# Kernel optimization log

Hardware: AMD Instinct MI355X
Metric: run time of the kernel (lower is better)

Reference implementation:

```python
import jax, jax.numpy as jnp
import numpy as np
from math import sqrt

D_MODEL = 1024
N_HEADS = 16
FF_MULT = 4
MAX_DIST = 512
LN_EPS = 1e-5


def layer_norm(x, g, b):
    mu = jnp.mean(x, axis=-1, keepdims=True)
    var = jnp.var(x, axis=-1, keepdims=True)
    return (x - mu) * jax.lax.rsqrt(var + LN_EPS) * g + b


def setup_inputs() -> dict:
    key = jax.random.key(0)
    ks = jax.random.split(key, 10)
    D, H, F = D_MODEL, N_HEADS, D_MODEL * FF_MULT
    s = 0.02
    return {
        "x": jax.random.normal(ks[0], (2, 2048, D), dtype=jnp.float32),
        "w_qkv": jax.random.normal(ks[1], (D, 3 * D), dtype=jnp.float32) * s,
        "b_qkv": jnp.zeros((3 * D,), jnp.float32),
        "w_out": jax.random.normal(ks[2], (D, D), dtype=jnp.float32) * s,
        "b_out": jnp.zeros((D,), jnp.float32),
        "rel_bias": jax.random.normal(ks[3], (2 * MAX_DIST + 1, H), dtype=jnp.float32) * s,
        "g1": jnp.ones((D,), jnp.float32),
        "beta1": jnp.zeros((D,), jnp.float32),
        "w1": jax.random.normal(ks[4], (D, F), dtype=jnp.float32) * s,
        "b1": jnp.zeros((F,), jnp.float32),
        "w2": jax.random.normal(ks[5], (F, D), dtype=jnp.float32) * s,
        "b2": jnp.zeros((D,), jnp.float32),
        "g2": jnp.ones((D,), jnp.float32),
        "beta2": jnp.zeros((D,), jnp.float32),
    }


def reference(x, w_qkv, b_qkv, w_out, b_out, rel_bias, g1, beta1, w1, b1, w2, b2, g2, beta2):
    B, T, D = x.shape
    H = N_HEADS
    hd = D // H
    qkv = x @ w_qkv + b_qkv                      # [B,T,3D]
    q, k, v = jnp.split(qkv, 3, axis=-1)
    # [B,H,T,hd]
    q = q.reshape(B, T, H, hd).transpose(0, 2, 1, 3)
    k = k.reshape(B, T, H, hd).transpose(0, 2, 1, 3)
    v = v.reshape(B, T, H, hd).transpose(0, 2, 1, 3)
    scores = jnp.einsum("bhqd,bhkd->bhqk", q, k) / sqrt(hd)
    # relative position bias: gather from table [2*max_dist+1, H]
    rel = jnp.clip(jnp.arange(T)[None, :] - jnp.arange(T)[:, None], -MAX_DIST, MAX_DIST) + MAX_DIST
    bias = rel_bias[rel].transpose(2, 0, 1)       # [H,T,T]
    attn = jax.nn.softmax(scores + bias[None], axis=-1)
    out = jnp.einsum("bhqk,bhkd->bhqd", attn, v).transpose(0, 2, 1, 3).reshape(B, T, D)
    out = out @ w_out + b_out                     # dropout inactive (eval)
    x2 = layer_norm(x + out, g1, beta1)
    ff = jax.nn.gelu(x2 @ w1 + b1, approximate=False) @ w2 + b2
    x3 = layer_norm(x2 + ff, g2, beta2)
    return (x3, attn)
```

## Files before the change

kernel.cpp:

```cpp
#include <hip/hip_runtime.h>
#include <hip/hip_bf16.h>
#include <cstdint>
#include <cstddef>

#define DEVFN static __device__ __forceinline__

typedef __attribute__((ext_vector_type(8))) short bf16x8;
typedef __attribute__((ext_vector_type(4))) float f32x4;

#define WAITVM(N) asm volatile("s_waitcnt vmcnt(" #N ")" ::: "memory")
#define WAITLGKM() asm volatile("s_waitcnt lgkmcnt(0)" ::: "memory")
#define BAR() __builtin_amdgcn_s_barrier()

DEVFN float exp2f_fast(float x) { return __builtin_amdgcn_exp2f(x); }

DEVFN ushort f2bf(float f) {
  uint32_t u = __float_as_uint(f);
  return (ushort)((u + 0x7fffu + ((u >> 16) & 1u)) >> 16);
}

DEVFN void gl_lds16(const void* g, void* l) {
  __builtin_amdgcn_global_load_lds(
      (const __attribute__((address_space(1))) void*)g,
      (__attribute__((address_space(3))) void*)l, 16, 0, 0);
}

DEVFN float wred_sum(float v) {
#pragma unroll
  for (int o = 32; o; o >>= 1) v += __shfl_xor(v, o);
  return v;
}


__global__ __launch_bounds__(256) void pack_bf16(const float* __restrict__ in,
                                                 ushort* __restrict__ out) {
  size_t i = ((size_t)blockIdx.x * 256 + threadIdx.x) * 4;
  float4 v = *(const float4*)&in[i];
  ushort4 u = make_ushort4(f2bf(v.x), f2bf(v.y), f2bf(v.z), f2bf(v.w));
  *(ushort4*)&out[i] = u;
}

__global__ __launch_bounds__(256) void wtrans(const float* __restrict__ in,
                                              ushort* __restrict__ out,
                                              int K, int N) {
  __shared__ float tile[32][33];
  int n0 = blockIdx.x * 32, k0 = blockIdx.y * 32;
  int tid = threadIdx.x;
#pragma unroll
  for (int i = 0; i < 4; ++i) {
    int idx = tid + i * 256;
    int r = idx >> 5, c = idx & 31;
    tile[r][c] = in[(size_t)(k0 + r) * N + n0 + c];
  }
  __syncthreads();
#pragma unroll
  for (int i = 0; i < 4; ++i) {
    int idx = tid + i * 256;
    int r = idx >> 5, c = idx & 31;
    out[(size_t)(n0 + r) * K + k0 + c] = f2bf(tile[c][r]);
  }
}

__global__ __launch_bounds__(256) void pack_vT(const ushort* __restrict__ qkv,
                                               ushort* __restrict__ vT) {
  __shared__ ushort tile[64][72];
  int bh = blockIdx.y, b = bh >> 4, h = bh & 15;
  int t0 = blockIdx.x * 64;
  int tid = threadIdx.x;
#pragma unroll
  for (int i = 0; i < 16; ++i) {
    int idx = tid + i * 256;
    int r = idx >> 6, c = idx & 63;
    tile[r][c] = qkv[(size_t)(b * 2048 + t0 + r) * 3072 + 2048 + h * 64 + c];
  }
  __syncthreads();
#pragma unroll
  for (int i = 0; i < 16; ++i) {
    int idx = tid + i * 256;
    int d = idx >> 6, t = idx & 63;
    vT[((size_t)bh * 64 + d) * 2048 + t0 + t] = tile[t][d];
  }
}


template <bool GELU, bool STF32, bool STBF16>
__global__ __launch_bounds__(256)
void gemm128(const ushort* __restrict__ A, int lda,
             const ushort* __restrict__ BT, int ldb,
             const float* __restrict__ bias,
             float* __restrict__ Cf, ushort* __restrict__ Cb, int ldc, int K,
             size_t cstride) {
  __shared__ ushort lsa[128 * 64];
  __shared__ ushort lsb[128 * 64];
  const int tid = threadIdx.x;
  const int lane = tid & 63;
  const int wv = tid >> 6;
  const int wr = (wv >> 1) * 64, wc = (wv & 1) * 64;
  const size_t kStart = (size_t)blockIdx.z * K;
  const ushort* Ab = A + (size_t)blockIdx.y * 128 * lda + kStart;
  const ushort* Bb = BT + (size_t)blockIdx.x * 128 * ldb + kStart;
  f32x4 acc[4][4] = {};
  int rowS[4], slotS[4];
#pragma unroll
  for (int i = 0; i < 4; ++i) {
    int idx = tid + i * 256;
    rowS[i] = idx >> 3;
    slotS[i] = (idx & 7) ^ (rowS[i] & 7);
  }
  for (int kt = 0; kt < K; kt += 64) {
    __syncthreads();
#pragma unroll
    for (int i = 0; i < 4; ++i) {
      gl_lds16(Ab + (size_t)rowS[i] * lda + kt + slotS[i] * 8, &lsa[(tid + i * 256) * 8]);
      gl_lds16(Bb + (size_t)rowS[i] * ldb + kt + slotS[i] * 8, &lsb[(tid + i * 256) * 8]);
    }
    asm volatile("s_waitcnt vmcnt(0)" ::: "memory");
    __syncthreads();
#pragma unroll
    for (int kk = 0; kk < 2; ++kk) {
      bf16x8 af[4], bfr[4];
      const int g = kk * 4 + (lane >> 4);
#pragma unroll
      for (int m = 0; m < 4; ++m) {
        int r = wr + m * 16 + (lane & 15);
        af[m] = *(const bf16x8*)&lsa[r * 64 + ((g ^ (r & 7)) * 8)];
      }
#pragma unroll
      for (int n = 0; n < 4; ++n) {
        int r = wc + n * 16 + (lane & 15);
        bfr[n] = *(const bf16x8*)&lsb[r * 64 + ((g ^ (r & 7)) * 8)];
      }
#pragma unroll
      for (int m = 0; m < 4; ++m)
#pragma unroll
        for (int n = 0; n < 4; ++n)
          acc[m][n] = __builtin_amdgcn_mfma_f32_16x16x32_bf16(af[m], bfr[n], acc[m][n], 0, 0, 0);
    }
  }
  const int rb = blockIdx.y * 128 + wr + ((lane >> 4) << 2);
  const int cb = blockIdx.x * 128 + wc + (lane & 15);
  float* Cfz = Cf + (size_t)blockIdx.z * cstride;
  ushort* Cbz = Cb + (size_t)blockIdx.z * cstride;
#pragma unroll
  for (int m = 0; m < 4; ++m)
#pragma unroll
    for (int n = 0; n < 4; ++n) {
      int col = cb + n * 16;
      float bv = bias ? bias[col] : 0.0f;
#pragma unroll
      for (int i = 0; i < 4; ++i) {
        int row = rb + m * 16 + i;
        float v = acc[m][n][i] + bv;
        if (GELU) v = 0.5f * v * (1.0f + erff(v * 0.70710678f));
        if (STF32) Cfz[(size_t)row * ldc + col] = v;
        if (STBF16) Cbz[(size_t)row * ldc + col] = f2bf(v);
      }
    }
}


DEVFN void attn_bid2(int& qb, int& bh, int& hf) {
  int lin = blockIdx.x;
  int xcd = lin & 7;
  int idx = lin >> 3;
  int orig = xcd * 128 + idx;
  hf = orig & 1;
  qb = (orig >> 1) & 15;
  bh = orig >> 5;
}

__global__ __launch_bounds__(256, 4)
void attn_den(const ushort* __restrict__ qkv, const float* __restrict__ rel_bias,
              float* __restrict__ lsum) {
  __shared__ ushort lsk[2][64 * 64];
  __shared__ float extb[1034];
  const int tid = threadIdx.x;
  const int lane = tid & 63;
  const int wv = tid >> 6;
  const int hi = lane >> 4;
  const int lo = lane & 15;
  int qb, bh, hf;
  attn_bid2(qb, bh, hf);
  const int b = bh >> 4, h = bh & 15;
  const int q0 = qb * 128;
  const int t0 = hf * 16;
  const ushort* qp = qkv + (size_t)b * 2048 * 3072 + h * 64;
  const ushort* kp = qp + 1024;
  const float C_SC = 0.18033688011f;
  ushort* lsq = (ushort*)lsk;

  for (int i = tid; i < 1034; i += 256) {
    int j = i - 3;
    j = j < 0 ? 0 : (j > 1024 ? 1024 : j);
    extb[i] = rel_bias[j * 16 + h] * 1.44269504f;
  }
#pragma unroll
  for (int i = 0; i < 4; ++i) {
    int idx = tid + i * 256;
    int row = idx >> 3;
    int slot = (idx & 7) ^ (row & 7);
    gl_lds16(qp + (size_t)(q0 + row) * 3072 + slot * 8, &lsq[idx * 8]);
  }
  WAITVM(0);
  WAITLGKM();
  BAR();
  bf16x8 qf[2][2];
#pragma unroll
  for (int mq = 0; mq < 2; ++mq)
#pragma unroll
    for (int kk = 0; kk < 2; ++kk) {
      int r = wv * 32 + mq * 16 + lo;
      int g = kk * 4 + hi;
      qf[mq][kk] = *(const bf16x8*)&lsq[r * 64 + ((g ^ (r & 7)) * 8)];
    }
  WAITLGKM();
  BAR();

  const int r0 = tid >> 3;
  const int sl0 = (tid & 7) ^ (r0 & 7);
  const int r1 = (tid + 256) >> 3;
  const int sl1 = ((tid + 256) & 7) ^ (r1 & 7);
  auto stageK = [&](int t, int buf) {
    gl_lds16(kp + (size_t)(t * 64 + r0) * 3072 + sl0 * 8, &lsk[buf][tid * 8]);
    gl_lds16(kp + (size_t)(t * 64 + r1) * 3072 + sl1 * 8, &lsk[buf][(tid + 256) * 8]);
  };

  float l_part[2] = {0.0f, 0.0f};
  stageK(t0, 0);
  for (int t = t0; t < t0 + 16; ++t) {
    if (t < t0 + 15) {
      stageK(t + 1, (t + 1) & 1);
      WAITVM(2);
    } else {
      WAITVM(0);
    }
    BAR();
    f32x4 sacc[4][2] = {};
    __builtin_amdgcn_s_setprio(1);
#pragma unroll
    for (int kk = 0; kk < 2; ++kk) {
      const int g = kk * 4 + hi;
      bf16x8 ak[4];
#pragma unroll
      for (int mk = 0; mk < 4; ++mk) {
        int r = mk * 16 + lo;
        ak[mk] = *(const bf16x8*)&lsk[t & 1][r * 64 + ((g ^ (r & 7)) * 8)];
      }
#pragma unroll
      for (int mk = 0; mk < 4; ++mk)
#pragma unroll
        for (int mq = 0; mq < 2; ++mq)
          sacc[mk][mq] =
              __builtin_amdgcn_mfma_f32_16x16x32_bf16(ak[mk], qf[mq][kk], sacc[mk][mq], 0, 0, 0);
    }
    __builtin_amdgcn_s_setprio(0);
    const bool farR = (t * 64) >= q0 + 640;
    const bool farL = (t * 64 + 63) <= q0 - 512;
    if (farR || farL) {
      const float bc = farR ? extb[3 + 1024] : extb[3];
#pragma unroll
      for (int mq = 0; mq < 2; ++mq) {
        float s = 0.0f;
#pragma unroll
        for (int mk = 0; mk < 4; ++mk)
#pragma unroll
          for (int i = 0; i < 4; ++i)
            s += exp2f_fast(fmaf(sacc[mk][mq][i], C_SC, bc));
        l_part[mq] += s;
      }
    } else {
      const int kbase = t * 64 + hi * 4;
      const int qr = q0 + wv * 32 + lo;
#pragma unroll
      for (int mq = 0; mq < 2; ++mq) {
        float s = 0.0f;
#pragma unroll
        for (int mk = 0; mk < 4; ++mk) {
          int k0 = (kbase + mk * 16) - (qr + mq * 16) + 515;
          k0 = k0 < 0 ? 0 : (k0 > 1030 ? 1030 : k0);
#pragma unroll
          for (int i = 0; i < 4; ++i)
            s += exp2f_fast(fmaf(sacc[mk][mq][i], C_SC, extb[k0 + i]));
        }
        l_part[mq] += s;
      }
    }
    BAR();
  }

#pragma unroll
  for (int mq = 0; mq < 2; ++mq) {
    float l = l_part[mq];
    l += __shfl_xor(l, 16);
    l += __shfl_xor(l, 32);
    if (hi == 0)
      lsum[(size_t)hf * 65536 + (size_t)bh * 2048 + q0 + wv * 32 + mq * 16 + lo] = l;
  }
}

__global__ __launch_bounds__(256, 3)
void attn_pv2(const ushort* __restrict__ qkv, const ushort* __restrict__ vT,
              const float* __restrict__ rel_bias, const float* __restrict__ lsum,
              float* __restrict__ attn, float* __restrict__ opart) {
  __shared__ ushort lsk[2][64 * 64];
  __shared__ ushort lsv[2][64 * 64];
  __shared__ ushort lsp[128 * 64];
  __shared__ float extb[1034];
  const int tid = threadIdx.x;
  const int lane = tid & 63;
  const int wv = tid >> 6;
  const int hi = lane >> 4;
  const int lo = lane & 15;
  int qb, bh, hf;
  attn_bid2(qb, bh, hf);
  const int b = bh >> 4, h = bh & 15;
  const int q0 = qb * 128;
  const int t0 = hf * 16;
  const ushort* qp = qkv + (size_t)b * 2048 * 3072 + h * 64;
  const ushort* kp = qp + 1024;
  const ushort* vp = vT + (size_t)bh * 64 * 2048;
  float* attnb = attn + (size_t)bh * 2048 * 2048;
  const float C_SC = 0.18033688011f;

  for (int i = tid; i < 1034; i += 256) {
    int j = i - 3;
    j = j < 0 ? 0 : (j > 1024 ? 1024 : j);
    extb[i] = rel_bias[j * 16 + h] * 1.44269504f;
  }
#pragma unroll
  for (int i = 0; i < 4; ++i) {
    int idx = tid + i * 256;
    int row = idx >> 3;
    int slot = (idx & 7) ^ (row & 7);
    gl_lds16(qp + (size_t)(q0 + row) * 3072 + slot * 8, &lsp[idx * 8]);
  }
  WAITVM(0);
  WAITLGKM();
  BAR();
  bf16x8 qf[2][2];
#pragma unroll
  for (int mq = 0; mq < 2; ++mq)
#pragma unroll
    for (int kk = 0; kk < 2; ++kk) {
      int r = wv * 32 + mq * 16 + lo;
      int g = kk * 4 + hi;
      qf[mq][kk] = *(const bf16x8*)&lsp[r * 64 + ((g ^ (r & 7)) * 8)];
    }
  WAITLGKM();
  BAR();

  float il[2];
#pragma unroll
  for (int mq = 0; mq < 2; ++mq) {
    size_t qi = (size_t)bh * 2048 + q0 + wv * 32 + mq * 16 + lo;
    il[mq] = 1.0f / (lsum[qi] + lsum[qi + 65536]);
  }

  const int r0 = tid >> 3;
  const int sl0 = (tid & 7) ^ (r0 & 7);
  const int r1 = (tid + 256) >> 3;
  const int sl1 = ((tid + 256) & 7) ^ (r1 & 7);
  auto stageK = [&](int t, int buf) {
    gl_lds16(kp + (size_t)(t * 64 + r0) * 3072 + sl0 * 8, &lsk[buf][tid * 8]);
    gl_lds16(kp + (size_t)(t * 64 + r1) * 3072 + sl1 * 8, &lsk[buf][(tid + 256) * 8]);
  };
  auto stageV = [&](int t, int buf) {
    gl_lds16(vp + (size_t)r0 * 2048 + t * 64 + sl0 * 8, &lsv[buf][tid * 8]);
    gl_lds16(vp + (size_t)r1 * 2048 + t * 64 + sl1 * 8, &lsv[buf][(tid + 256) * 8]);
  };

  f32x4 acc_o[2][4] = {};
  stageK(t0, 0);
  stageV(t0, 0);
  for (int t = t0; t < t0 + 16; ++t) {
    if (t < t0 + 15) {
      stageK(t + 1, (t + 1) & 1);
      stageV(t + 1, (t + 1) & 1);
    }
    if (t == t0) { WAITVM(4); }
    else if (t < t0 + 15) { WAITVM(12); }
    else { WAITVM(8); }
    BAR();
    f32x4 sacc[4][2] = {};
    __builtin_amdgcn_s_setprio(1);
#pragma unroll
    for (int kk = 0; kk < 2; ++kk) {
      const int g = kk * 4 + hi;
      bf16x8 ak[4];
#pragma unroll
      for (int mk = 0; mk < 4; ++mk) {
        int r = mk * 16 + lo;
        ak[mk] = *(const bf16x8*)&lsk[t & 1][r * 64 + ((g ^ (r & 7)) * 8)];
      }
#pragma unroll
      for (int mk = 0; mk < 4; ++mk)
#pragma unroll
        for (int mq = 0; mq < 2; ++mq)
          sacc[mk][mq] =
              __builtin_amdgcn_mfma_f32_16x16x32_bf16(ak[mk], qf[mq][kk], sacc[mk][mq], 0, 0, 0);
    }
    __builtin_amdgcn_s_setprio(0);
    const bool farR = (t * 64) >= q0 + 640;
    const bool farT = farR || ((t * 64 + 63) <= q0 - 512);
    const float bcf = farR ? extb[3 + 1024] : extb[3];
#pragma unroll
    for (int mq = 0; mq < 2; ++mq) {
      const int row = wv * 32 + mq * 16 + lo;
      const float l = il[mq];
#pragma unroll
      for (int mk = 0; mk < 4; ++mk) {
        const int c0 = mk * 16 + hi * 4;
        float p4[4];
        if (farT) {
#pragma unroll
          for (int i = 0; i < 4; ++i)
            p4[i] = exp2f_fast(fmaf(sacc[mk][mq][i], C_SC, bcf)) * l;
        } else {
          int k0 = (t * 64 + c0) - (q0 + row) + 515;
          k0 = k0 < 0 ? 0 : (k0 > 1030 ? 1030 : k0);
#pragma unroll
          for (int i = 0; i < 4; ++i)
            p4[i] = exp2f_fast(fmaf(sacc[mk][mq][i], C_SC, extb[k0 + i])) * l;
        }
        ushort4 u = make_ushort4(f2bf(p4[0]), f2bf(p4[1]), f2bf(p4[2]), f2bf(p4[3]));
        *(ushort4*)&lsp[row * 64 + (((c0 >> 3) ^ (row & 7)) << 3) + (c0 & 7)] = u;
        *(float4*)&attnb[(size_t)(q0 + row) * 2048 + t * 64 + c0] =
            make_float4(p4[0], p4[1], p4[2], p4[3]);
      }
    }
    WAITLGKM();
    BAR();
    __builtin_amdgcn_s_setprio(1);
#pragma unroll
    for (int kk = 0; kk < 2; ++kk) {
      const int g = kk * 4 + hi;
      bf16x8 ap[2], bv2[4];
#pragma unroll
      for (int m = 0; m < 2; ++m) {
        int r = wv * 32 + m * 16 + lo;
        ap[m] = *(const bf16x8*)&lsp[r * 64 + ((g ^ (r & 7)) * 8)];
      }
#pragma unroll
      for (int n = 0; n < 4; ++n) {
        int r = n * 16 + lo;
        bv2[n] = *(const bf16x8*)&lsv[t & 1][r * 64 + ((g ^ (r & 7)) * 8)];
      }
#pragma unroll
      for (int m = 0; m < 2; ++m)
#pragma unroll
        for (int n = 0; n < 4; ++n)
          acc_o[m][n] = __builtin_amdgcn_mfma_f32_16x16x32_bf16(ap[m], bv2[n], acc_o[m][n], 0, 0, 0);
    }
    __builtin_amdgcn_s_setprio(0);
  }

  float* ob = opart + (size_t)hf * 4194304;
#pragma unroll
  for (int m = 0; m < 2; ++m)
#pragma unroll
    for (int n = 0; n < 4; ++n) {
      int col = h * 64 + n * 16 + lo;
#pragma unroll
      for (int i = 0; i < 4; ++i) {
        int row = q0 + wv * 32 + m * 16 + (hi << 2) + i;
        ob[(size_t)(b * 2048 + row) * 1024 + col] = acc_o[m][n][i];
      }
    }
}

__global__ __launch_bounds__(256) void ocomb(const float* __restrict__ opart,
                                             ushort* __restrict__ ctx) {
  size_t i = ((size_t)blockIdx.x * 256 + threadIdx.x) * 4;
  float4 a = *(const float4*)&opart[i];
  float4 c = *(const float4*)&opart[4194304 + i];
  ushort4 u = make_ushort4(f2bf(a.x + c.x), f2bf(a.y + c.y),
                           f2bf(a.z + c.z), f2bf(a.w + c.w));
  *(ushort4*)&ctx[i] = u;
}


__global__ __launch_bounds__(256)
void add_ln(const float* __restrict__ a, const float* __restrict__ r0,
            const float* __restrict__ r1, const float* __restrict__ bias,
            const float* __restrict__ g, const float* __restrict__ be,
            float* __restrict__ outf, ushort* __restrict__ outb) {
  const int tid = threadIdx.x;
  const size_t base = (size_t)blockIdx.x * 1024 + tid * 4;
  float4 va = *(const float4*)&a[base];
  float4 vr = *(const float4*)&r0[base];
  float x0 = va.x + vr.x, x1 = va.y + vr.y, x2 = va.z + vr.z, x3 = va.w + vr.w;
  if (r1) {
    float4 v1 = *(const float4*)&r1[base];
    x0 += v1.x; x1 += v1.y; x2 += v1.z; x3 += v1.w;
  }
  if (bias) {
    float4 vb4 = *(const float4*)&bias[tid * 4];
    x0 += vb4.x; x1 += vb4.y; x2 += vb4.z; x3 += vb4.w;
  }
  float s = x0 + x1 + x2 + x3;
  float s2 = x0 * x0 + x1 * x1 + x2 * x2 + x3 * x3;
  s = wred_sum(s);
  s2 = wred_sum(s2);
  __shared__ float rs[4], rq[4];
  if ((tid & 63) == 0) { rs[tid >> 6] = s; rq[tid >> 6] = s2; }
  __syncthreads();
  s = rs[0] + rs[1] + rs[2] + rs[3];
  s2 = rq[0] + rq[1] + rq[2] + rq[3];
  const float mean = s * (1.0f / 1024.0f);
  const float var = s2 * (1.0f / 1024.0f) - mean * mean;
  const float sc = rsqrtf(var + 1e-5f);
  float4 vg = *(const float4*)&g[tid * 4];
  float4 vb = *(const float4*)&be[tid * 4];
  float y0 = (x0 - mean) * sc * vg.x + vb.x;
  float y1 = (x1 - mean) * sc * vg.y + vb.y;
  float y2 = (x2 - mean) * sc * vg.z + vb.z;
  float y3 = (x3 - mean) * sc * vg.w + vb.w;
  *(float4*)&outf[base] = make_float4(y0, y1, y2, y3);
  if (outb) {
    ushort4 u = make_ushort4(f2bf(y0), f2bf(y1), f2bf(y2), f2bf(y3));
    *(ushort4*)&outb[base] = u;
  }
}


extern "C" void kernel_launch(void* const* d_in, const int* in_sizes, int n_in,
                              void* d_out, int out_size, void* d_ws, size_t ws_size,
                              hipStream_t stream) {
  const float* x     = (const float*)d_in[0];
  const float* w_qkv = (const float*)d_in[1];
  const float* b_qkv = (const float*)d_in[2];
  const float* w_out = (const float*)d_in[3];
  const float* b_out = (const float*)d_in[4];
  const float* relb  = (const float*)d_in[5];
  const float* g1    = (const float*)d_in[6];
  const float* be1   = (const float*)d_in[7];
  const float* w1    = (const float*)d_in[8];
  const float* b1    = (const float*)d_in[9];
  const float* w2    = (const float*)d_in[10];
  const float* b2    = (const float*)d_in[11];
  const float* g2    = (const float*)d_in[12];
  const float* be2   = (const float*)d_in[13];

  float* x3o  = (float*)d_out;
  float* attn = x3o + (size_t)4194304;

  char* w = (char*)d_ws;
  size_t off = 0;
  auto alloc = [&](size_t bytes) {
    void* p = w + off;
    off += (bytes + 255) & ~(size_t)255;
    return p;
  };
  ushort* x_bf   = (ushort*)alloc(4096ull * 1024 * 2);
  ushort* wqkvT  = (ushort*)alloc(3072ull * 1024 * 2);
  ushort* woutT  = (ushort*)alloc(1024ull * 1024 * 2);
  ushort* w1T    = (ushort*)alloc(4096ull * 1024 * 2);
  ushort* w2T    = (ushort*)alloc(1024ull * 4096 * 2);
  ushort* qkv_bf = (ushort*)alloc(4096ull * 3072 * 2);
  ushort* vT     = (ushort*)alloc(32ull * 64 * 2048 * 2);
  ushort* ctx_bf = (ushort*)alloc(4096ull * 1024 * 2);
  float*  lsum   = (float*)alloc(2ull * 32 * 2048 * 4);
  float*  opart  = (float*)alloc(2ull * 4096 * 1024 * 4);
  float*  p0     = (float*)alloc(4096ull * 1024 * 4);
  float*  p1     = (float*)alloc(4096ull * 1024 * 4);
  float*  x2f    = (float*)alloc(4096ull * 1024 * 4);
  ushort* x2bf   = (ushort*)alloc(4096ull * 1024 * 2);
  ushort* ff1_bf = (ushort*)alloc(4096ull * 4096 * 2);

  pack_bf16<<<4096, 256, 0, stream>>>(x, x_bf);
  wtrans<<<dim3(96, 32), 256, 0, stream>>>(w_qkv, wqkvT, 1024, 3072);
  wtrans<<<dim3(32, 32), 256, 0, stream>>>(w_out, woutT, 1024, 1024);
  wtrans<<<dim3(128, 32), 256, 0, stream>>>(w1, w1T, 1024, 4096);
  wtrans<<<dim3(32, 128), 256, 0, stream>>>(w2, w2T, 4096, 1024);

  gemm128<false, false, true><<<dim3(24, 32), 256, 0, stream>>>(
      x_bf, 1024, wqkvT, 1024, b_qkv, nullptr, qkv_bf, 3072, 1024, 0);
  attn_den<<<1024, 256, 0, stream>>>(qkv_bf, relb, lsum);
  pack_vT<<<dim3(32, 32), 256, 0, stream>>>(qkv_bf, vT);
  attn_pv2<<<1024, 256, 0, stream>>>(qkv_bf, vT, relb, lsum, attn, opart);
  ocomb<<<4096, 256, 0, stream>>>(opart, ctx_bf);

  gemm128<false, true, false><<<dim3(8, 32, 2), 256, 0, stream>>>(
      ctx_bf, 1024, woutT, 1024, nullptr, p0, nullptr, 1024, 512,
      (size_t)(p1 - p0));
  add_ln<<<4096, 256, 0, stream>>>(x, p0, p1, b_out, g1, be1, x2f, x2bf);
  gemm128<true, false, true><<<dim3(32, 32), 256, 0, stream>>>(
      x2bf, 1024, w1T, 1024, b1, nullptr, ff1_bf, 4096, 1024, 0);
  gemm128<false, true, false><<<dim3(8, 32, 2), 256, 0, stream>>>(
      ff1_bf, 4096, w2T, 4096, nullptr, p0, nullptr, 1024, 2048,
      (size_t)(p1 - p0));
  add_ln<<<4096, 256, 0, stream>>>(x2f, p0, p1, b2, g2, be2, x3o, nullptr);
}
```

Baseline: 451.1 us.

## Merge prep kernels, fold V transpose into attn_den, store partial outputs as bf16

Folds the x conversion and the four weight transposes into one prep launch. The V transpose now runs as extra blocks inside the attention-denominator kernel, and attn_pv2 writes its two partial outputs in bf16 instead of fp32. These cut launch count and halve the opart write and read traffic. In exchange, partial outputs are rounded to bf16 before they are summed, and attn_den_vt carries an extra shared tile that may lower its occupancy.

```diff
diff --git a/kernel.cpp b/kernel.cpp
--- a/kernel.cpp
+++ b/kernel.cpp
@@ -18,6 +18,7 @@
   uint32_t u = __float_as_uint(f);
   return (ushort)((u + 0x7fffu + ((u >> 16) & 1u)) >> 16);
 }
+DEVFN float bf2f(ushort u) { return __uint_as_float((uint32_t)u << 16); }
 
 DEVFN void gl_lds16(const void* g, void* l) {
   __builtin_amdgcn_global_load_lds(
@@ -32,53 +33,50 @@
 }
 
 
-__global__ __launch_bounds__(256) void pack_bf16(const float* __restrict__ in,
-                                                 ushort* __restrict__ out) {
-  size_t i = ((size_t)blockIdx.x * 256 + threadIdx.x) * 4;
-  float4 v = *(const float4*)&in[i];
-  ushort4 u = make_ushort4(f2bf(v.x), f2bf(v.y), f2bf(v.z), f2bf(v.w));
-  *(ushort4*)&out[i] = u;
-}
-
-__global__ __launch_bounds__(256) void wtrans(const float* __restrict__ in,
-                                              ushort* __restrict__ out,
-                                              int K, int N) {
-  __shared__ float tile[32][33];
-  int n0 = blockIdx.x * 32, k0 = blockIdx.y * 32;
-  int tid = threadIdx.x;
+DEVFN void wtrans_body(const float* __restrict__ in, ushort* __restrict__ out,
+                       int K, int N, int bx, int by, int tid, float* tile ) {
+  int n0 = bx * 32, k0 = by * 32;
 #pragma unroll
   for (int i = 0; i < 4; ++i) {
     int idx = tid + i * 256;
     int r = idx >> 5, c = idx & 31;
-    tile[r][c] = in[(size_t)(k0 + r) * N + n0 + c];
+    tile[r * 33 + c] = in[(size_t)(k0 + r) * N + n0 + c];
   }
   __syncthreads();
 #pragma unroll
   for (int i = 0; i < 4; ++i) {
     int idx = tid + i * 256;
     int r = idx >> 5, c = idx & 31;
-    out[(size_t)(n0 + r) * K + k0 + c] = f2bf(tile[c][r]);
-  }
-}
-
-__global__ __launch_bounds__(256) void pack_vT(const ushort* __restrict__ qkv,
-                                               ushort* __restrict__ vT) {
-  __shared__ ushort tile[64][72];
-  int bh = blockIdx.y, b = bh >> 4, h = bh & 15;
-  int t0 = blockIdx.x * 64;
-  int tid = threadIdx.x;
-#pragma unroll
-  for (int i = 0; i < 16; ++i) {
-    int idx = tid + i * 256;
-    int r = idx >> 6, c = idx & 63;
-    tile[r][c] = qkv[(size_t)(b * 2048 + t0 + r) * 3072 + 2048 + h * 64 + c];
-  }
-  __syncthreads();
-#pragma unroll
-  for (int i = 0; i < 16; ++i) {
-    int idx = tid + i * 256;
-    int d = idx >> 6, t = idx & 63;
-    vT[((size_t)bh * 64 + d) * 2048 + t0 + t] = tile[t][d];
+    out[(size_t)(n0 + r) * K + k0 + c] = f2bf(tile[c * 33 + r]);
+  }
+}
+
+__global__ __launch_bounds__(256)
+void prep(const float* __restrict__ x, ushort* __restrict__ x_bf,
+          const float* __restrict__ w_qkv, ushort* __restrict__ wqkvT,
+          const float* __restrict__ w1, ushort* __restrict__ w1T,
+          const float* __restrict__ w2, ushort* __restrict__ w2T,
+          const float* __restrict__ w_out, ushort* __restrict__ woutT) {
+  __shared__ float tile[32 * 33];
+  const int blk = blockIdx.x;
+  const int tid = threadIdx.x;
+  if (blk < 4096) {
+    size_t i = ((size_t)blk * 256 + tid) * 4;
+    float4 v = *(const float4*)&x[i];
+    ushort4 u = make_ushort4(f2bf(v.x), f2bf(v.y), f2bf(v.z), f2bf(v.w));
+    *(ushort4*)&x_bf[i] = u;
+  } else if (blk < 7168) {
+    int j = blk - 4096;
+    wtrans_body(w_qkv, wqkvT, 1024, 3072, j % 96, j / 96, tid, tile);
+  } else if (blk < 11264) {
+    int j = blk - 7168;
+    wtrans_body(w1, w1T, 1024, 4096, j & 127, j >> 7, tid, tile);
+  } else if (blk < 15360) {
+    int j = blk - 11264;
+    wtrans_body(w2, w2T, 4096, 1024, j & 31, j >> 5, tid, tile);
+  } else {
+    int j = blk - 15360;
+    wtrans_body(w_out, woutT, 1024, 1024, j & 31, j >> 5, tid, tile);
   }
 }
 
@@ -170,11 +168,34 @@
 }
 
 __global__ __launch_bounds__(256, 4)
-void attn_den(const ushort* __restrict__ qkv, const float* __restrict__ rel_bias,
-              float* __restrict__ lsum) {
+void attn_den_vt(const ushort* __restrict__ qkv, const float* __restrict__ rel_bias,
+                 float* __restrict__ lsum, ushort* __restrict__ vT) {
   __shared__ ushort lsk[2][64 * 64];
   __shared__ float extb[1034];
+  __shared__ ushort vtile[64][72];
   const int tid = threadIdx.x;
+
+  if (blockIdx.x >= 1024) {
+    int j = blockIdx.x - 1024;
+    int t0v = (j & 31) * 64;
+    int bhv = j >> 5;
+    int bv = bhv >> 4, hv = bhv & 15;
+#pragma unroll
+    for (int i = 0; i < 16; ++i) {
+      int idx = tid + i * 256;
+      int r = idx >> 6, c = idx & 63;
+      vtile[r][c] = qkv[(size_t)(bv * 2048 + t0v + r) * 3072 + 2048 + hv * 64 + c];
+    }
+    __syncthreads();
+#pragma unroll
+    for (int i = 0; i < 16; ++i) {
+      int idx = tid + i * 256;
+      int d = idx >> 6, t = idx & 63;
+      vT[((size_t)bhv * 64 + d) * 2048 + t0v + t] = vtile[t][d];
+    }
+    return;
+  }
+
   const int lane = tid & 63;
   const int wv = tid >> 6;
   const int hi = lane >> 4;
@@ -301,7 +322,7 @@
 __global__ __launch_bounds__(256, 3)
 void attn_pv2(const ushort* __restrict__ qkv, const ushort* __restrict__ vT,
               const float* __restrict__ rel_bias, const float* __restrict__ lsum,
-              float* __restrict__ attn, float* __restrict__ opart) {
+              float* __restrict__ attn, ushort* __restrict__ opart) {
   __shared__ ushort lsk[2][64 * 64];
   __shared__ ushort lsv[2][64 * 64];
   __shared__ ushort lsp[128 * 64];
@@ -454,7 +475,7 @@
     __builtin_amdgcn_s_setprio(0);
   }
 
-  float* ob = opart + (size_t)hf * 4194304;
+  ushort* ob = opart + (size_t)hf * 4194304;
 #pragma unroll
   for (int m = 0; m < 2; ++m)
 #pragma unroll
@@ -463,18 +484,18 @@
 #pragma unroll
       for (int i = 0; i < 4; ++i) {
         int row = q0 + wv * 32 + m * 16 + (hi << 2) + i;
-        ob[(size_t)(b * 2048 + row) * 1024 + col] = acc_o[m][n][i];
-      }
-    }
-}
-
-__global__ __launch_bounds__(256) void ocomb(const float* __restrict__ opart,
+        ob[(size_t)(b * 2048 + row) * 1024 + col] = f2bf(acc_o[m][n][i]);
+      }
+    }
+}
+
+__global__ __launch_bounds__(256) void ocomb(const ushort* __restrict__ opart,
                                              ushort* __restrict__ ctx) {
   size_t i = ((size_t)blockIdx.x * 256 + threadIdx.x) * 4;
-  float4 a = *(const float4*)&opart[i];
-  float4 c = *(const float4*)&opart[4194304 + i];
-  ushort4 u = make_ushort4(f2bf(a.x + c.x), f2bf(a.y + c.y),
-                           f2bf(a.z + c.z), f2bf(a.w + c.w));
+  ushort4 a = *(const ushort4*)&opart[i];
+  ushort4 c = *(const ushort4*)&opart[4194304 + i];
+  ushort4 u = make_ushort4(f2bf(bf2f(a.x) + bf2f(c.x)), f2bf(bf2f(a.y) + bf2f(c.y)),
+                           f2bf(bf2f(a.z) + bf2f(c.z)), f2bf(bf2f(a.w) + bf2f(c.w)));
   *(ushort4*)&ctx[i] = u;
 }
 
@@ -560,23 +581,18 @@
   ushort* vT     = (ushort*)alloc(32ull * 64 * 2048 * 2);
   ushort* ctx_bf = (ushort*)alloc(4096ull * 1024 * 2);
   float*  lsum   = (float*)alloc(2ull * 32 * 2048 * 4);
-  float*  opart  = (float*)alloc(2ull * 4096 * 1024 * 4);
+  ushort* opart  = (ushort*)alloc(2ull * 4096 * 1024 * 2);
   float*  p0     = (float*)alloc(4096ull * 1024 * 4);
   float*  p1     = (float*)alloc(4096ull * 1024 * 4);
   float*  x2f    = (float*)alloc(4096ull * 1024 * 4);
   ushort* x2bf   = (ushort*)alloc(4096ull * 1024 * 2);
   ushort* ff1_bf = (ushort*)alloc(4096ull * 4096 * 2);
 
-  pack_bf16<<<4096, 256, 0, stream>>>(x, x_bf);
-  wtrans<<<dim3(96, 32), 256, 0, stream>>>(w_qkv, wqkvT, 1024, 3072);
-  wtrans<<<dim3(32, 32), 256, 0, stream>>>(w_out, woutT, 1024, 1024);
-  wtrans<<<dim3(128, 32), 256, 0, stream>>>(w1, w1T, 1024, 4096);
-  wtrans<<<dim3(32, 128), 256, 0, stream>>>(w2, w2T, 4096, 1024);
-
+  prep<<<16384, 256, 0, stream>>>(x, x_bf, w_qkv, wqkvT, w1, w1T, w2, w2T,
+                                  w_out, woutT);
   gemm128<false, false, true><<<dim3(24, 32), 256, 0, stream>>>(
       x_bf, 1024, wqkvT, 1024, b_qkv, nullptr, qkv_bf, 3072, 1024, 0);
-  attn_den<<<1024, 256, 0, stream>>>(qkv_bf, relb, lsum);
-  pack_vT<<<dim3(32, 32), 256, 0, stream>>>(qkv_bf, vT);
+  attn_den_vt<<<2048, 256, 0, stream>>>(qkv_bf, relb, lsum, vT);
   attn_pv2<<<1024, 256, 0, stream>>>(qkv_bf, vT, relb, lsum, attn, opart);
   ocomb<<<4096, 256, 0, stream>>>(opart, ctx_bf);
 
```

Measured after the change: 433.3 us. -3.9%, faster.
